# Optimization experiments

Hardware: AMD Instinct MI355X
Metric: run time of the kernel (lower is better)

## Reference

```python
import jax, jax.numpy as jnp
import numpy as np
import math

C = 512
D = C // 4  # 128
SCALE = math.sqrt(D)

def setup_inputs() -> dict:
    key = jax.random.key(0)
    k1, k2, k3, k4 = jax.random.split(key, 4)
    x = jax.random.normal(k1, (8, C, 2048), dtype=jnp.float32)
    # q_conv and k_conv share the same weight (tied in the torch module)
    wqk = jax.random.normal(k2, (D, C), dtype=jnp.float32) * (1.0 / math.sqrt(C))
    wv = jax.random.normal(k3, (D, C), dtype=jnp.float32) * (1.0 / math.sqrt(C))
    bv = jax.random.normal(k4, (D,), dtype=jnp.float32) * 0.01
    return {"x": x, "wqk": wqk, "wv": wv, "bv": bv}

def reference(x, wqk, wv, bv):
    # x: [B, C, N]; 1x1 conv == matmul over channel dim
    xq = jnp.einsum('dc,bcn->bnd', wqk, x)          # [B, N, D]
    xk = jnp.einsum('dc,bcn->bdn', wqk, x)          # [B, D, N]
    xv = jnp.einsum('dc,bcn->bdn', wv, x) + bv[None, :, None]  # [B, D, N]
    energy = jnp.einsum('bnd,bdm->bnm', xq, xk) / SCALE  # [B, N, N]
    attention = jax.nn.softmax(energy, axis=-1)
    x_r = jnp.einsum('bdn,bnm->bdm', xv, attention)  # [B, D, N]
    return x_r
```

## Files before the change

### kernel.cpp

```cpp
#include <hip/hip_runtime.h>

typedef short short4v __attribute__((ext_vector_type(4)));
typedef short short8 __attribute__((ext_vector_type(8)));
typedef float floatx4 __attribute__((ext_vector_type(4)));
typedef unsigned int uint;
typedef unsigned short ushort;

#define CH 512
#define NN 2048
#define DD 128
#define RSCALE 0.08838834764831845f

__device__ __forceinline__ float bf2f(ushort u) {
    union { uint i; float f; } v; v.i = ((uint)u) << 16; return v.f;
}
__device__ __forceinline__ ushort f2bf(float f) {
    union { float f; uint u; } v; v.f = f;
    uint u = v.u;
    return (ushort)((u + 0x7fffu + ((u >> 16) & 1u)) >> 16);
}

__global__ __launch_bounds__(256) void k0_prep(
    const float* __restrict__ wqk, const float* __restrict__ wv,
    ushort* __restrict__ Wbf, float* __restrict__ lsum)
{
    int gid = blockIdx.x * 256 + threadIdx.x;
    int base = gid * 4;
    const float* src = (base < 65536) ? (wqk + base) : (wv + base - 65536);
    float4 v = *(const float4*)src;
    short4v o;
    o[0] = (short)f2bf(v.x); o[1] = (short)f2bf(v.y);
    o[2] = (short)f2bf(v.z); o[3] = (short)f2bf(v.w);
    *(short4v*)&Wbf[base] = o;
    if (gid < 16384) lsum[gid] = 0.0f;
}

__global__ __launch_bounds__(256) void k1_proj(
    const float* __restrict__ x,
    const ushort* __restrict__ Wbf,
    const float* __restrict__ bv,
    ushort* __restrict__ Q,
    ushort* __restrict__ V)
{
    const int nt = blockIdx.x;
    const int b  = blockIdx.y;
    const int n0 = nt * 32;
    const int t = threadIdx.x;
    const int lane = t & 63, w = t >> 6, l15 = lane & 15, quad = lane >> 4;

    __shared__ __attribute__((aligned(16))) ushort As[32 * 40];
    __shared__ __attribute__((aligned(16))) ushort Bs[256 * 40];

    floatx4 acc[2][4];
#pragma unroll
    for (int i = 0; i < 2; i++)
#pragma unroll
        for (int j = 0; j < 4; j++) acc[i][j] = (floatx4)(0.0f);

    const float* xb = x + b * (CH * NN) + n0;

    for (int c0 = 0; c0 < CH; c0 += 32) {
        {
            int n = t & 31, g = t >> 5;
            short4v v;
#pragma unroll
            for (int i = 0; i < 4; i++)
                v[i] = (short)f2bf(xb[(c0 + g * 4 + i) * NN + n]);
            *(short4v*)&As[n * 40 + g * 4] = v;
        }
#pragma unroll
        for (int rep = 0; rep < 16; rep++) {
            int idx = rep * 256 + t;
            int row = idx >> 4, cp = idx & 15;
            *(uint*)&Bs[row * 40 + cp * 2] = *(const uint*)&Wbf[row * CH + c0 + cp * 2];
        }
        __syncthreads();
        short8 a0 = *(short8*)&As[(l15) * 40 + quad * 8];
        short8 a1 = *(short8*)&As[(16 + l15) * 40 + quad * 8];
#pragma unroll
        for (int dt2 = 0; dt2 < 4; dt2++) {
            short8 bf = *(short8*)&Bs[(w * 64 + dt2 * 16 + l15) * 40 + quad * 8];
            acc[0][dt2] = __builtin_amdgcn_mfma_f32_16x16x32_bf16(a0, bf, acc[0][dt2], 0, 0, 0);
            acc[1][dt2] = __builtin_amdgcn_mfma_f32_16x16x32_bf16(a1, bf, acc[1][dt2], 0, 0, 0);
        }
        __syncthreads();
    }
#pragma unroll
    for (int ns = 0; ns < 2; ns++)
#pragma unroll
        for (int dt2 = 0; dt2 < 4; dt2++) {
            int ds_ = w * 64 + dt2 * 16 + l15;
#pragma unroll
            for (int r = 0; r < 4; r++) {
                int n = n0 + ns * 16 + quad * 4 + r;
                float val = acc[ns][dt2][r];
                if (ds_ < 128) {
                    Q[b * (NN * DD) + n * DD + ds_] = f2bf(val);
                } else {
                    int dv = ds_ - 128;
                    V[b * (NN * DD) + n * DD + dv] = f2bf(val + bv[dv]);
                }
            }
        }
}

__global__ __launch_bounds__(256) void kl_sum(
    const ushort* __restrict__ Q,
    float* __restrict__ lsum)
{
    int pid = blockIdx.x;
    const int b = blockIdx.y;
    int it = 0;
    while (pid >= (16 - it)) { pid -= (16 - it); it++; }
    const int jt = it + pid;
    const int i0 = it * 128, j0 = jt * 128;
    const int t = threadIdx.x;
    const int lane = t & 63, w = t >> 6, l15 = lane & 15, quad = lane >> 4;
    const int wi = (w >> 1) * 64, wj = (w & 1) * 64;

    __shared__ __attribute__((aligned(16))) ushort Qi[128 * 136];
    __shared__ __attribute__((aligned(16))) ushort Qj[128 * 136];

    const ushort* Qb = Q + b * (NN * DD);

#pragma unroll
    for (int rep = 0; rep < 8; rep++) {
        int idx = rep * 256 + t;
        int row = idx >> 4, g = idx & 15;
        *(short8*)&Qi[row * 136 + g * 8] = *(const short8*)&Qb[(i0 + row) * DD + g * 8];
        *(short8*)&Qj[row * 136 + g * 8] = *(const short8*)&Qb[(j0 + row) * DD + g * 8];
    }
    __syncthreads();

    floatx4 acc[4][4];
#pragma unroll
    for (int i = 0; i < 4; i++)
#pragma unroll
        for (int j = 0; j < 4; j++) acc[i][j] = (floatx4)(0.0f);

#pragma unroll
    for (int kd = 0; kd < 4; kd++) {
        short8 afr[4], bfr[4];
#pragma unroll
        for (int nt = 0; nt < 4; nt++)
            afr[nt] = *(short8*)&Qi[(wi + nt * 16 + l15) * 136 + kd * 32 + quad * 8];
#pragma unroll
        for (int mt = 0; mt < 4; mt++)
            bfr[mt] = *(short8*)&Qj[(wj + mt * 16 + l15) * 136 + kd * 32 + quad * 8];
#pragma unroll
        for (int nt = 0; nt < 4; nt++)
#pragma unroll
            for (int mt = 0; mt < 4; mt++)
                acc[nt][mt] = __builtin_amdgcn_mfma_f32_16x16x32_bf16(afr[nt], bfr[mt], acc[nt][mt], 0, 0, 0);
    }

    float cs[4] = {0.f, 0.f, 0.f, 0.f};
#pragma unroll
    for (int nt = 0; nt < 4; nt++) {
        float rs[4] = {0.f, 0.f, 0.f, 0.f};
#pragma unroll
        for (int mt = 0; mt < 4; mt++)
#pragma unroll
            for (int r = 0; r < 4; r++) {
                float p = __expf(acc[nt][mt][r] * RSCALE);
                rs[r] += p;
                cs[mt] += p;
            }
#pragma unroll
        for (int r = 0; r < 4; r++) {
            float s = rs[r];
            s += __shfl_xor(s, 1);
            s += __shfl_xor(s, 2);
            s += __shfl_xor(s, 4);
            s += __shfl_xor(s, 8);
            if (l15 == 0)
                atomicAdd(&lsum[b * NN + i0 + wi + nt * 16 + quad * 4 + r], s);
        }
    }
    if (it != jt) {
#pragma unroll
        for (int mt = 0; mt < 4; mt++) {
            float s = cs[mt];
            s += __shfl_xor(s, 16);
            s += __shfl_xor(s, 32);
            if (lane < 16)
                atomicAdd(&lsum[b * NN + j0 + wj + mt * 16 + l15], s);
        }
    }
}

__global__ __launch_bounds__(256) void k2_scale_t(
    const ushort* __restrict__ V,
    const float* __restrict__ lsum,
    ushort* __restrict__ VT)
{
    const int nt = blockIdx.x;
    const int b = blockIdx.y;
    const int n0 = nt * 64;
    const int t = threadIdx.x;

    __shared__ __attribute__((aligned(16))) ushort Vt[64 * 132];

    const ushort* Vb = V + b * (NN * DD);
#pragma unroll
    for (int rep = 0; rep < 16; rep++) {
        int idx = rep * 256 + t;
        int row = idx >> 6, dp = idx & 63;
        *(uint*)&Vt[row * 132 + dp * 2] = *(const uint*)&Vb[(n0 + row) * DD + dp * 2];
    }
    __syncthreads();
#pragma unroll
    for (int rep = 0; rep < 16; rep++) {
        int idx = rep * 256 + t;
        int d = idx >> 5, col2 = idx & 31;
        int n = n0 + col2 * 2;
        float l0 = 1.0f / lsum[b * NN + n], l1 = 1.0f / lsum[b * NN + n + 1];
        float v0 = bf2f(Vt[(col2 * 2) * 132 + d]) * l0;
        float v1 = bf2f(Vt[(col2 * 2 + 1) * 132 + d]) * l1;
        uint pack = (uint)f2bf(v0) | ((uint)f2bf(v1) << 16);
        *(uint*)&VT[(size_t)b * DD * NN + (size_t)d * NN + n] = pack;
    }
}

__global__ __launch_bounds__(256) void k_fused(
    const ushort* __restrict__ Q,
    const ushort* __restrict__ VT,
    float* __restrict__ part)
{
    const int mt = blockIdx.x;
    const int h  = blockIdx.y;
    const int b  = blockIdx.z;
    const int m0 = mt * 64;
    const int t = threadIdx.x;
    const int lane = t & 63, w = t >> 6, l15 = lane & 15, quad = lane >> 4;

    __shared__ __attribute__((aligned(16))) ushort Qm[64 * 136];
    __shared__ __attribute__((aligned(16))) ushort Qn[64 * 136];
    __shared__ __attribute__((aligned(16))) ushort Vs[128 * 72];
    __shared__ __attribute__((aligned(16))) ushort Ps[64 * 68];

    const ushort* Qb = Q + b * (NN * DD);
    const ushort* VTb = VT + (size_t)b * DD * NN;

#pragma unroll
    for (int rep = 0; rep < 4; rep++) {
        int idx = rep * 256 + t;
        int row = idx >> 4, g = idx & 15;
        *(short8*)&Qm[row * 136 + g * 8] = *(const short8*)&Qb[(m0 + row) * DD + g * 8];
    }
    __syncthreads();

    short8 qm[4][4];
#pragma unroll
    for (int ms = 0; ms < 4; ms++)
#pragma unroll
        for (int kd = 0; kd < 4; kd++)
            qm[ms][kd] = *(short8*)&Qm[(ms * 16 + l15) * 136 + kd * 32 + quad * 8];

    floatx4 acc[2][4];
#pragma unroll
    for (int i = 0; i < 2; i++)
#pragma unroll
        for (int j = 0; j < 4; j++) acc[i][j] = (floatx4)(0.0f);

    const int nbeg = h * (NN / 2), nend = nbeg + (NN / 2);
    for (int n0c = nbeg; n0c < nend; n0c += 64) {
        __syncthreads();
#pragma unroll
        for (int rep = 0; rep < 4; rep++) {
            int idx = rep * 256 + t;
            int row = idx >> 4, g = idx & 15;
            *(short8*)&Qn[row * 136 + g * 8] = *(const short8*)&Qb[(n0c + row) * DD + g * 8];
        }
#pragma unroll
        for (int rep = 0; rep < 4; rep++) {
            int idx = rep * 256 + t;
            int d = idx >> 3, g = idx & 7;
            *(short8*)&Vs[d * 72 + g * 8] = *(const short8*)&VTb[(size_t)d * NN + n0c + g * 8];
        }
        __syncthreads();

        {
            short8 bq[4];
#pragma unroll
            for (int kd = 0; kd < 4; kd++)
                bq[kd] = *(short8*)&Qn[(w * 16 + l15) * 136 + kd * 32 + quad * 8];
#pragma unroll
            for (int ms = 0; ms < 4; ms++) {
                floatx4 s = (floatx4)(0.0f);
#pragma unroll
                for (int kd = 0; kd < 4; kd++)
                    s = __builtin_amdgcn_mfma_f32_16x16x32_bf16(qm[ms][kd], bq[kd], s, 0, 0, 0);
#pragma unroll
                for (int r = 0; r < 4; r++) {
                    float p = __expf(s[r] * RSCALE);
                    Ps[(ms * 16 + quad * 4 + r) * 68 + w * 16 + l15] = f2bf(p);
                }
            }
        }
        __syncthreads();

#pragma unroll
        for (int kn = 0; kn < 2; kn++) {
            short8 va0 = *(short8*)&Vs[(w * 32 + l15) * 72 + kn * 32 + quad * 8];
            short8 va1 = *(short8*)&Vs[(w * 32 + 16 + l15) * 72 + kn * 32 + quad * 8];
#pragma unroll
            for (int mf = 0; mf < 4; mf++) {
                short8 pb = *(short8*)&Ps[(mf * 16 + l15) * 68 + kn * 32 + quad * 8];
                acc[0][mf] = __builtin_amdgcn_mfma_f32_16x16x32_bf16(va0, pb, acc[0][mf], 0, 0, 0);
                acc[1][mf] = __builtin_amdgcn_mfma_f32_16x16x32_bf16(va1, pb, acc[1][mf], 0, 0, 0);
            }
        }
    }

    float* ob = part + (size_t)h * (8 * DD * NN) + (size_t)b * DD * NN;
#pragma unroll
    for (int dsub = 0; dsub < 2; dsub++)
#pragma unroll
        for (int mf = 0; mf < 4; mf++)
#pragma unroll
            for (int r = 0; r < 4; r++) {
                int d = w * 32 + dsub * 16 + quad * 4 + r;
                ob[(size_t)d * NN + m0 + mf * 16 + l15] = acc[dsub][mf][r];
            }
}

__global__ __launch_bounds__(256) void k_reduce(
    const float* __restrict__ part, float* __restrict__ out)
{
    int gid = blockIdx.x * 256 + threadIdx.x;
    const size_t half = (size_t)8 * DD * NN;
    float4 a = *(const float4*)&part[gid * 4];
    float4 b = *(const float4*)&part[half + gid * 4];
    float4 o;
    o.x = a.x + b.x; o.y = a.y + b.y; o.z = a.z + b.z; o.w = a.w + b.w;
    *(float4*)&out[gid * 4] = o;
}

__global__ __launch_bounds__(256) void k1_fb(
    const float* __restrict__ x, const float* __restrict__ wqk,
    const float* __restrict__ wv, const float* __restrict__ bv,
    ushort* __restrict__ Q, ushort* __restrict__ V)
{
    const int nt = blockIdx.x;
    const int b  = blockIdx.y;
    const int n0 = nt * 32;
    const int t = threadIdx.x;
    const int lane = t & 63, w = t >> 6, l15 = lane & 15, quad = lane >> 4;

    __shared__ __attribute__((aligned(16))) ushort As[32 * 40];
    __shared__ __attribute__((aligned(16))) ushort Bs[256 * 40];

    floatx4 acc[2][4];
#pragma unroll
    for (int i = 0; i < 2; i++)
#pragma unroll
        for (int j = 0; j < 4; j++) acc[i][j] = (floatx4)(0.0f);

    const float* xb = x + b * (CH * NN) + n0;

    for (int c0 = 0; c0 < CH; c0 += 32) {
        {
            int n = t & 31, g = t >> 5;
            short4v v;
#pragma unroll
            for (int i = 0; i < 4; i++)
                v[i] = (short)f2bf(xb[(c0 + g * 4 + i) * NN + n]);
            *(short4v*)&As[n * 40 + g * 4] = v;
        }
#pragma unroll
        for (int rep = 0; rep < 16; rep++) {
            int idx = rep * 256 + t;
            int row = idx >> 4, cp = idx & 15;
            const float* wf = (row < 128) ? (wqk + row * CH) : (wv + (row - 128) * CH);
            uint pack = (uint)f2bf(wf[c0 + cp * 2]) | ((uint)f2bf(wf[c0 + cp * 2 + 1]) << 16);
            *(uint*)&Bs[row * 40 + cp * 2] = pack;
        }
        __syncthreads();
        short8 a0 = *(short8*)&As[(l15) * 40 + quad * 8];
        short8 a1 = *(short8*)&As[(16 + l15) * 40 + quad * 8];
#pragma unroll
        for (int dt2 = 0; dt2 < 4; dt2++) {
            short8 bf = *(short8*)&Bs[(w * 64 + dt2 * 16 + l15) * 40 + quad * 8];
            acc[0][dt2] = __builtin_amdgcn_mfma_f32_16x16x32_bf16(a0, bf, acc[0][dt2], 0, 0, 0);
            acc[1][dt2] = __builtin_amdgcn_mfma_f32_16x16x32_bf16(a1, bf, acc[1][dt2], 0, 0, 0);
        }
        __syncthreads();
    }
#pragma unroll
    for (int ns = 0; ns < 2; ns++)
#pragma unroll
        for (int dt2 = 0; dt2 < 4; dt2++) {
            int ds_ = w * 64 + dt2 * 16 + l15;
#pragma unroll
            for (int r = 0; r < 4; r++) {
                int n = n0 + ns * 16 + quad * 4 + r;
                float val = acc[ns][dt2][r];
                if (ds_ < 128) {
                    Q[b * (NN * DD) + n * DD + ds_] = f2bf(val);
                } else {
                    int dv = ds_ - 128;
                    V[b * (NN * DD) + n * DD + dv] = f2bf(val + bv[dv]);
                }
            }
        }
}

__global__ __launch_bounds__(256) void k2_norm(
    const ushort* __restrict__ Q, ushort* __restrict__ V)
{
    const int ntile = blockIdx.x;
    const int b = blockIdx.y;
    const int n0 = ntile * 64;
    const int t = threadIdx.x;
    const int lane = t & 63, w = t >> 6, l15 = lane & 15, quad = lane >> 4;

    __shared__ __attribute__((aligned(16))) ushort Qs[64 * 136];
    __shared__ __attribute__((aligned(16))) ushort Qm2[64 * 136];

    const ushort* Qb = Q + b * (NN * DD);

#pragma unroll
    for (int rep = 0; rep < 16; rep++) {
        int idx = rep * 256 + t;
        int row = idx >> 6, dp = idx & 63;
        *(uint*)&Qs[row * 136 + dp * 2] = *(const uint*)&Qb[(n0 + row) * DD + dp * 2];
    }
    __syncthreads();

    short8 afr[4];
#pragma unroll
    for (int kd = 0; kd < 4; kd++)
        afr[kd] = *(short8*)&Qs[(w * 16 + l15) * 136 + kd * 32 + quad * 8];

    float sums[4] = {0.f, 0.f, 0.f, 0.f};

    for (int m0 = 0; m0 < NN; m0 += 64) {
#pragma unroll
        for (int rep = 0; rep < 16; rep++) {
            int idx = rep * 256 + t;
            int row = idx >> 6, dp = idx & 63;
            *(uint*)&Qm2[row * 136 + dp * 2] = *(const uint*)&Qb[(m0 + row) * DD + dp * 2];
        }
        __syncthreads();
#pragma unroll
        for (int ct = 0; ct < 4; ct++) {
            floatx4 s = (floatx4)(0.0f);
#pragma unroll
            for (int kd = 0; kd < 4; kd++) {
                short8 bf = *(short8*)&Qm2[(ct * 16 + l15) * 136 + kd * 32 + quad * 8];
                s = __builtin_amdgcn_mfma_f32_16x16x32_bf16(afr[kd], bf, s, 0, 0, 0);
            }
#pragma unroll
            for (int r = 0; r < 4; r++)
                sums[r] += __expf(s[r] * RSCALE);
        }
        __syncthreads();
    }

#pragma unroll
    for (int r = 0; r < 4; r++) {
        float s = sums[r];
        s += __shfl_xor(s, 1);
        s += __shfl_xor(s, 2);
        s += __shfl_xor(s, 4);
        s += __shfl_xor(s, 8);
        sums[r] = s;
    }

    ushort* Vb = V + b * (NN * DD);
#pragma unroll
    for (int r = 0; r < 4; r++) {
        int n = n0 + w * 16 + quad * 4 + r;
        float inv = 1.0f / sums[r];
        short8 vv = *(short8*)&Vb[n * DD + l15 * 8];
        short8 o;
#pragma unroll
        for (int i = 0; i < 8; i++)
            o[i] = (short)f2bf(bf2f((ushort)vv[i]) * inv);
        *(short8*)&Vb[n * DD + l15 * 8] = o;
    }
}

__global__ __launch_bounds__(256) void k3_attn(
    const ushort* __restrict__ Q, const ushort* __restrict__ Vp,
    float* __restrict__ out)
{
    const int mtile = blockIdx.x;
    const int b = blockIdx.y;
    const int m0 = mtile * 64;
    const int t = threadIdx.x;
    const int lane = t & 63, w = t >> 6, l15 = lane & 15, quad = lane >> 4;

    __shared__ __attribute__((aligned(16))) ushort Qs[64 * 136];
    __shared__ __attribute__((aligned(16))) ushort Qn2[32 * 136];
    __shared__ __attribute__((aligned(16))) ushort Vs2[128 * 40];
    __shared__ __attribute__((aligned(16))) ushort Ps2[64 * 40];

    const ushort* Qb = Q + b * (NN * DD);
    const ushort* Vpb = Vp + b * (NN * DD);

#pragma unroll
    for (int rep = 0; rep < 16; rep++) {
        int idx = rep * 256 + t;
        int row = idx >> 6, dp = idx & 63;
        *(uint*)&Qs[row * 136 + dp * 2] = *(const uint*)&Qb[(m0 + row) * DD + dp * 2];
    }
    __syncthreads();

    short8 afr[4];
#pragma unroll
    for (int kd = 0; kd < 4; kd++)
        afr[kd] = *(short8*)&Qs[(w * 16 + l15) * 136 + kd * 32 + quad * 8];

    floatx4 acc[2][4];
#pragma unroll
    for (int s = 0; s < 2; s++)
#pragma unroll
        for (int mt = 0; mt < 4; mt++) acc[s][mt] = (floatx4)(0.0f);

    for (int n0c = 0; n0c < NN; n0c += 32) {
#pragma unroll
        for (int rep = 0; rep < 8; rep++) {
            int idx = rep * 256 + t;
            int row = idx >> 6, dp = idx & 63;
            *(uint*)&Qn2[row * 136 + dp * 2] = *(const uint*)&Qb[(n0c + row) * DD + dp * 2];
        }
#pragma unroll
        for (int rep = 0; rep < 8; rep++) {
            int idx = rep * 256 + t;
            int np = idx >> 7, d = idx & 127;
            uint v0 = Vpb[(n0c + np * 2) * DD + d];
            uint v1 = Vpb[(n0c + np * 2 + 1) * DD + d];
            *(uint*)&Vs2[d * 40 + np * 2] = v0 | (v1 << 16);
        }
        __syncthreads();

#pragma unroll
        for (int nt2 = 0; nt2 < 2; nt2++) {
            floatx4 s = (floatx4)(0.0f);
#pragma unroll
            for (int kd = 0; kd < 4; kd++) {
                short8 bf = *(short8*)&Qn2[(nt2 * 16 + l15) * 136 + kd * 32 + quad * 8];
                s = __builtin_amdgcn_mfma_f32_16x16x32_bf16(afr[kd], bf, s, 0, 0, 0);
            }
#pragma unroll
            for (int r = 0; r < 4; r++) {
                float p = __expf(s[r] * RSCALE);
                Ps2[(w * 16 + quad * 4 + r) * 40 + nt2 * 16 + l15] = f2bf(p);
            }
        }
        __syncthreads();

        short8 pb[4];
#pragma unroll
        for (int mt = 0; mt < 4; mt++)
            pb[mt] = *(short8*)&Ps2[(mt * 16 + l15) * 40 + quad * 8];
#pragma unroll
        for (int sub = 0; sub < 2; sub++) {
            short8 va = *(short8*)&Vs2[(w * 32 + sub * 16 + l15) * 40 + quad * 8];
#pragma unroll
            for (int mt = 0; mt < 4; mt++)
                acc[sub][mt] = __builtin_amdgcn_mfma_f32_16x16x32_bf16(va, pb[mt], acc[sub][mt], 0, 0, 0);
        }
        __syncthreads();
    }

    float* ob = out + (size_t)b * DD * NN;
#pragma unroll
    for (int sub = 0; sub < 2; sub++)
#pragma unroll
        for (int mt = 0; mt < 4; mt++)
#pragma unroll
            for (int r = 0; r < 4; r++) {
                int d = w * 32 + sub * 16 + quad * 4 + r;
                int m = m0 + mt * 16 + l15;
                ob[(size_t)d * NN + m] = acc[sub][mt][r];
            }
}

extern "C" void kernel_launch(void* const* d_in, const int* in_sizes, int n_in,
                              void* d_out, int out_size, void* d_ws, size_t ws_size,
                              hipStream_t stream) {
    const float* x   = (const float*)d_in[0];
    const float* wqk = (const float*)d_in[1];
    const float* wv  = (const float*)d_in[2];
    const float* bv  = (const float*)d_in[3];
    float* out = (float*)d_out;

    ushort* Q = (ushort*)d_ws;
    ushort* V = (ushort*)((char*)d_ws + (4u << 20));

    if (ws_size >= (size_t)33 * 1024 * 1024) {
        ushort* Wbf  = (ushort*)((char*)d_ws + (8u << 20));
        float*  lsum = (float*)((char*)d_ws + (8u << 20) + (256u << 10));
        ushort* VT   = (ushort*)((char*)d_ws + (12u << 20));
        float*  part = (float*)((char*)d_ws + (16u << 20));

        k0_prep<<<128, 256, 0, stream>>>(wqk, wv, Wbf, lsum);
        k1_proj<<<dim3(64, 8), 256, 0, stream>>>(x, Wbf, bv, Q, V);
        kl_sum<<<dim3(136, 8), 256, 0, stream>>>(Q, lsum);
        k2_scale_t<<<dim3(32, 8), 256, 0, stream>>>(V, lsum, VT);
        k_fused<<<dim3(32, 2, 8), 256, 0, stream>>>(Q, VT, part);
        k_reduce<<<2048, 256, 0, stream>>>(part, out);
    } else {
        k1_fb<<<dim3(64, 8), 256, 0, stream>>>(x, wqk, wv, bv, Q, V);
        k2_norm<<<dim3(32, 8), 256, 0, stream>>>(Q, V);
        k3_attn<<<dim3(32, 8), 256, 0, stream>>>(Q, V, out);
    }
}
```

Measured before the change: 156.5 us.

## Write V transposed from projection and fold softmax normalization into fused attention

Result: faster. 152.2 us (-2.7%).

```diff
diff --git a/kernel.cpp b/kernel.cpp
--- a/kernel.cpp
+++ b/kernel.cpp
@@ -40,7 +40,7 @@
     const ushort* __restrict__ Wbf,
     const float* __restrict__ bv,
     ushort* __restrict__ Q,
-    ushort* __restrict__ V)
+    ushort* __restrict__ VT)
 {
     const int nt = blockIdx.x;
     const int b  = blockIdx.y;
@@ -50,6 +50,7 @@
 
     __shared__ __attribute__((aligned(16))) ushort As[32 * 40];
     __shared__ __attribute__((aligned(16))) ushort Bs[256 * 40];
+    __shared__ __attribute__((aligned(16))) ushort Vt[128 * 40];
 
     floatx4 acc[2][4];
 #pragma unroll
@@ -69,10 +70,292 @@
             *(short4v*)&As[n * 40 + g * 4] = v;
         }
 #pragma unroll
+        for (int rep = 0; rep < 4; rep++) {
+            int idx = rep * 256 + t;
+            int row = idx >> 2, g = idx & 3;
+            *(short8*)&Bs[row * 40 + g * 8] = *(const short8*)&Wbf[row * CH + c0 + g * 8];
+        }
+        __syncthreads();
+        short8 a0 = *(short8*)&As[(l15) * 40 + quad * 8];
+        short8 a1 = *(short8*)&As[(16 + l15) * 40 + quad * 8];
+#pragma unroll
+        for (int dt2 = 0; dt2 < 4; dt2++) {
+            short8 bf = *(short8*)&Bs[(w * 64 + dt2 * 16 + l15) * 40 + quad * 8];
+            acc[0][dt2] = __builtin_amdgcn_mfma_f32_16x16x32_bf16(a0, bf, acc[0][dt2], 0, 0, 0);
+            acc[1][dt2] = __builtin_amdgcn_mfma_f32_16x16x32_bf16(a1, bf, acc[1][dt2], 0, 0, 0);
+        }
+        __syncthreads();
+    }
+
+#pragma unroll
+    for (int ns = 0; ns < 2; ns++)
+#pragma unroll
+        for (int dt2 = 0; dt2 < 4; dt2++) {
+            int ds_ = w * 64 + dt2 * 16 + l15;
+#pragma unroll
+            for (int r = 0; r < 4; r++) {
+                int nl = ns * 16 + quad * 4 + r;
+                float val = acc[ns][dt2][r];
+                if (ds_ < 128) {
+                    Q[b * (NN * DD) + (n0 + nl) * DD + ds_] = f2bf(val);
+                } else {
+                    int dv = ds_ - 128;
+                    Vt[dv * 40 + nl] = f2bf(val + bv[dv]);
+                }
+            }
+        }
+    __syncthreads();
+#pragma unroll
+    for (int rep = 0; rep < 2; rep++) {
+        int idx = rep * 256 + t;
+        int dv = idx >> 2, seg = idx & 3;
+        *(short8*)&VT[((size_t)b * DD + dv) * NN + n0 + seg * 8] =
+            *(short8*)&Vt[dv * 40 + seg * 8];
+    }
+}
+
+__global__ __launch_bounds__(256) void kl_sum(
+    const ushort* __restrict__ Q,
+    float* __restrict__ lsum)
+{
+    int pid = blockIdx.x;
+    const int b = blockIdx.y;
+    int it = 0;
+    while (pid >= (16 - it)) { pid -= (16 - it); it++; }
+    const int jt = it + pid;
+    const int i0 = it * 128, j0 = jt * 128;
+    const int t = threadIdx.x;
+    const int lane = t & 63, w = t >> 6, l15 = lane & 15, quad = lane >> 4;
+    const int wi = (w >> 1) * 64, wj = (w & 1) * 64;
+
+    __shared__ __attribute__((aligned(16))) ushort Qi[128 * 136];
+    __shared__ __attribute__((aligned(16))) ushort Qj[128 * 136];
+
+    const ushort* Qb = Q + b * (NN * DD);
+
+#pragma unroll
+    for (int rep = 0; rep < 8; rep++) {
+        int idx = rep * 256 + t;
+        int row = idx >> 4, g = idx & 15;
+        *(short8*)&Qi[row * 136 + g * 8] = *(const short8*)&Qb[(i0 + row) * DD + g * 8];
+        *(short8*)&Qj[row * 136 + g * 8] = *(const short8*)&Qb[(j0 + row) * DD + g * 8];
+    }
+    __syncthreads();
+
+    floatx4 acc[4][4];
+#pragma unroll
+    for (int i = 0; i < 4; i++)
+#pragma unroll
+        for (int j = 0; j < 4; j++) acc[i][j] = (floatx4)(0.0f);
+
+#pragma unroll
+    for (int kd = 0; kd < 4; kd++) {
+        short8 afr[4], bfr[4];
+#pragma unroll
+        for (int nt = 0; nt < 4; nt++)
+            afr[nt] = *(short8*)&Qi[(wi + nt * 16 + l15) * 136 + kd * 32 + quad * 8];
+#pragma unroll
+        for (int mt = 0; mt < 4; mt++)
+            bfr[mt] = *(short8*)&Qj[(wj + mt * 16 + l15) * 136 + kd * 32 + quad * 8];
+#pragma unroll
+        for (int nt = 0; nt < 4; nt++)
+#pragma unroll
+            for (int mt = 0; mt < 4; mt++)
+                acc[nt][mt] = __builtin_amdgcn_mfma_f32_16x16x32_bf16(afr[nt], bfr[mt], acc[nt][mt], 0, 0, 0);
+    }
+
+    float cs[4] = {0.f, 0.f, 0.f, 0.f};
+#pragma unroll
+    for (int nt = 0; nt < 4; nt++) {
+        float rs[4] = {0.f, 0.f, 0.f, 0.f};
+#pragma unroll
+        for (int mt = 0; mt < 4; mt++)
+#pragma unroll
+            for (int r = 0; r < 4; r++) {
+                float p = __expf(acc[nt][mt][r] * RSCALE);
+                rs[r] += p;
+                cs[mt] += p;
+            }
+#pragma unroll
+        for (int r = 0; r < 4; r++) {
+            float s = rs[r];
+            s += __shfl_xor(s, 1);
+            s += __shfl_xor(s, 2);
+            s += __shfl_xor(s, 4);
+            s += __shfl_xor(s, 8);
+            if (l15 == 0)
+                atomicAdd(&lsum[b * NN + i0 + wi + nt * 16 + quad * 4 + r], s);
+        }
+    }
+    if (it != jt) {
+#pragma unroll
+        for (int mt = 0; mt < 4; mt++) {
+            float s = cs[mt];
+            s += __shfl_xor(s, 16);
+            s += __shfl_xor(s, 32);
+            if (lane < 16)
+                atomicAdd(&lsum[b * NN + j0 + wj + mt * 16 + l15], s);
+        }
+    }
+}
+
+__global__ __launch_bounds__(256) void k_fused(
+    const ushort* __restrict__ Q,
+    const ushort* __restrict__ VT,
+    const float* __restrict__ lsum,
+    float* __restrict__ part)
+{
+    const int mt = blockIdx.x;
+    const int h  = blockIdx.y;
+    const int b  = blockIdx.z;
+    const int m0 = mt * 64;
+    const int t = threadIdx.x;
+    const int lane = t & 63, w = t >> 6, l15 = lane & 15, quad = lane >> 4;
+
+    __shared__ __attribute__((aligned(16))) ushort Qm[64 * 136];
+    __shared__ __attribute__((aligned(16))) ushort Qn[64 * 136];
+    __shared__ __attribute__((aligned(16))) ushort Vs[128 * 72];
+    __shared__ __attribute__((aligned(16))) ushort Ps[64 * 68];
+
+    const ushort* Qb = Q + b * (NN * DD);
+    const ushort* VTb = VT + (size_t)b * DD * NN;
+    const float* lb = lsum + b * NN;
+
+#pragma unroll
+    for (int rep = 0; rep < 4; rep++) {
+        int idx = rep * 256 + t;
+        int row = idx >> 4, g = idx & 15;
+        *(short8*)&Qm[row * 136 + g * 8] = *(const short8*)&Qb[(m0 + row) * DD + g * 8];
+    }
+    __syncthreads();
+
+    short8 qm[4][4];
+#pragma unroll
+    for (int ms = 0; ms < 4; ms++)
+#pragma unroll
+        for (int kd = 0; kd < 4; kd++)
+            qm[ms][kd] = *(short8*)&Qm[(ms * 16 + l15) * 136 + kd * 32 + quad * 8];
+
+    floatx4 acc[2][4];
+#pragma unroll
+    for (int i = 0; i < 2; i++)
+#pragma unroll
+        for (int j = 0; j < 4; j++) acc[i][j] = (floatx4)(0.0f);
+
+    const int nbeg = h * (NN / 2), nend = nbeg + (NN / 2);
+    for (int n0c = nbeg; n0c < nend; n0c += 64) {
+        float lw = lb[n0c + w * 16 + l15];
+        __syncthreads();
+#pragma unroll
+        for (int rep = 0; rep < 4; rep++) {
+            int idx = rep * 256 + t;
+            int row = idx >> 4, g = idx & 15;
+            *(short8*)&Qn[row * 136 + g * 8] = *(const short8*)&Qb[(n0c + row) * DD + g * 8];
+        }
+#pragma unroll
+        for (int rep = 0; rep < 4; rep++) {
+            int idx = rep * 256 + t;
+            int d = idx >> 3, g = idx & 7;
+            *(short8*)&Vs[d * 72 + g * 8] = *(const short8*)&VTb[(size_t)d * NN + n0c + g * 8];
+        }
+        __syncthreads();
+
+        {
+            float linv = 1.0f / lw;
+            short8 bq[4];
+#pragma unroll
+            for (int kd = 0; kd < 4; kd++)
+                bq[kd] = *(short8*)&Qn[(w * 16 + l15) * 136 + kd * 32 + quad * 8];
+#pragma unroll
+            for (int ms = 0; ms < 4; ms++) {
+                floatx4 s = (floatx4)(0.0f);
+#pragma unroll
+                for (int kd = 0; kd < 4; kd++)
+                    s = __builtin_amdgcn_mfma_f32_16x16x32_bf16(qm[ms][kd], bq[kd], s, 0, 0, 0);
+#pragma unroll
+                for (int r = 0; r < 4; r++) {
+                    float p = __expf(s[r] * RSCALE) * linv;
+                    Ps[(ms * 16 + quad * 4 + r) * 68 + w * 16 + l15] = f2bf(p);
+                }
+            }
+        }
+        __syncthreads();
+
+#pragma unroll
+        for (int kn = 0; kn < 2; kn++) {
+            short8 va0 = *(short8*)&Vs[(w * 32 + l15) * 72 + kn * 32 + quad * 8];
+            short8 va1 = *(short8*)&Vs[(w * 32 + 16 + l15) * 72 + kn * 32 + quad * 8];
+#pragma unroll
+            for (int mf = 0; mf < 4; mf++) {
+                short8 pb = *(short8*)&Ps[(mf * 16 + l15) * 68 + kn * 32 + quad * 8];
+                acc[0][mf] = __builtin_amdgcn_mfma_f32_16x16x32_bf16(va0, pb, acc[0][mf], 0, 0, 0);
+                acc[1][mf] = __builtin_amdgcn_mfma_f32_16x16x32_bf16(va1, pb, acc[1][mf], 0, 0, 0);
+            }
+        }
+    }
+
+    float* ob = part + (size_t)h * (8 * DD * NN) + (size_t)b * DD * NN;
+#pragma unroll
+    for (int dsub = 0; dsub < 2; dsub++)
+#pragma unroll
+        for (int mf = 0; mf < 4; mf++)
+#pragma unroll
+            for (int r = 0; r < 4; r++) {
+                int d = w * 32 + dsub * 16 + quad * 4 + r;
+                ob[(size_t)d * NN + m0 + mf * 16 + l15] = acc[dsub][mf][r];
+            }
+}
+
+__global__ __launch_bounds__(256) void k_reduce(
+    const float* __restrict__ part, float* __restrict__ out)
+{
+    int gid = blockIdx.x * 256 + threadIdx.x;
+    const size_t half = (size_t)8 * DD * NN;
+    float4 a = *(const float4*)&part[gid * 4];
+    float4 b = *(const float4*)&part[half + gid * 4];
+    float4 o;
+    o.x = a.x + b.x; o.y = a.y + b.y; o.z = a.z + b.z; o.w = a.w + b.w;
+    *(float4*)&out[gid * 4] = o;
+}
+
+__global__ __launch_bounds__(256) void k1_fb(
+    const float* __restrict__ x, const float* __restrict__ wqk,
+    const float* __restrict__ wv, const float* __restrict__ bv,
+    ushort* __restrict__ Q, ushort* __restrict__ V)
+{
+    const int nt = blockIdx.x;
+    const int b  = blockIdx.y;
+    const int n0 = nt * 32;
+    const int t = threadIdx.x;
+    const int lane = t & 63, w = t >> 6, l15 = lane & 15, quad = lane >> 4;
+
+    __shared__ __attribute__((aligned(16))) ushort As[32 * 40];
+    __shared__ __attribute__((aligned(16))) ushort Bs[256 * 40];
+
+    floatx4 acc[2][4];
+#pragma unroll
+    for (int i = 0; i < 2; i++)
+#pragma unroll
+        for (int j = 0; j < 4; j++) acc[i][j] = (floatx4)(0.0f);
+
+    const float* xb = x + b * (CH * NN) + n0;
+
+    for (int c0 = 0; c0 < CH; c0 += 32) {
+        {
+            int n = t & 31, g = t >> 5;
+            short4v v;
+#pragma unroll
+            for (int i = 0; i < 4; i++)
+                v[i] = (short)f2bf(xb[(c0 + g * 4 + i) * NN + n]);
+            *(short4v*)&As[n * 40 + g * 4] = v;
+        }
+#pragma unroll
         for (int rep = 0; rep < 16; rep++) {
             int idx = rep * 256 + t;
             int row = idx >> 4, cp = idx & 15;
-            *(uint*)&Bs[row * 40 + cp * 2] = *(const uint*)&Wbf[row * CH + c0 + cp * 2];
+            const float* wf = (row < 128) ? (wqk + row * CH) : (wv + (row - 128) * CH);
+            uint pack = (uint)f2bf(wf[c0 + cp * 2]) | ((uint)f2bf(wf[c0 + cp * 2 + 1]) << 16);
+            *(uint*)&Bs[row * 40 + cp * 2] = pack;
         }
         __syncthreads();
         short8 a0 = *(short8*)&As[(l15) * 40 + quad * 8];
@@ -104,308 +387,6 @@
         }
 }
 
-__global__ __launch_bounds__(256) void kl_sum(
-    const ushort* __restrict__ Q,
-    float* __restrict__ lsum)
-{
-    int pid = blockIdx.x;
-    const int b = blockIdx.y;
-    int it = 0;
-    while (pid >= (16 - it)) { pid -= (16 - it); it++; }
-    const int jt = it + pid;
-    const int i0 = it * 128, j0 = jt * 128;
-    const int t = threadIdx.x;
-    const int lane = t & 63, w = t >> 6, l15 = lane & 15, quad = lane >> 4;
-    const int wi = (w >> 1) * 64, wj = (w & 1) * 64;
-
-    __shared__ __attribute__((aligned(16))) ushort Qi[128 * 136];
-    __shared__ __attribute__((aligned(16))) ushort Qj[128 * 136];
-
-    const ushort* Qb = Q + b * (NN * DD);
-
-#pragma unroll
-    for (int rep = 0; rep < 8; rep++) {
-        int idx = rep * 256 + t;
-        int row = idx >> 4, g = idx & 15;
-        *(short8*)&Qi[row * 136 + g * 8] = *(const short8*)&Qb[(i0 + row) * DD + g * 8];
-        *(short8*)&Qj[row * 136 + g * 8] = *(const short8*)&Qb[(j0 + row) * DD + g * 8];
-    }
-    __syncthreads();
-
-    floatx4 acc[4][4];
-#pragma unroll
-    for (int i = 0; i < 4; i++)
-#pragma unroll
-        for (int j = 0; j < 4; j++) acc[i][j] = (floatx4)(0.0f);
-
-#pragma unroll
-    for (int kd = 0; kd < 4; kd++) {
-        short8 afr[4], bfr[4];
-#pragma unroll
-        for (int nt = 0; nt < 4; nt++)
-            afr[nt] = *(short8*)&Qi[(wi + nt * 16 + l15) * 136 + kd * 32 + quad * 8];
-#pragma unroll
-        for (int mt = 0; mt < 4; mt++)
-            bfr[mt] = *(short8*)&Qj[(wj + mt * 16 + l15) * 136 + kd * 32 + quad * 8];
-#pragma unroll
-        for (int nt = 0; nt < 4; nt++)
-#pragma unroll
-            for (int mt = 0; mt < 4; mt++)
-                acc[nt][mt] = __builtin_amdgcn_mfma_f32_16x16x32_bf16(afr[nt], bfr[mt], acc[nt][mt], 0, 0, 0);
-    }
-
-    float cs[4] = {0.f, 0.f, 0.f, 0.f};
-#pragma unroll
-    for (int nt = 0; nt < 4; nt++) {
-        float rs[4] = {0.f, 0.f, 0.f, 0.f};
-#pragma unroll
-        for (int mt = 0; mt < 4; mt++)
-#pragma unroll
-            for (int r = 0; r < 4; r++) {
-                float p = __expf(acc[nt][mt][r] * RSCALE);
-                rs[r] += p;
-                cs[mt] += p;
-            }
-#pragma unroll
-        for (int r = 0; r < 4; r++) {
-            float s = rs[r];
-            s += __shfl_xor(s, 1);
-            s += __shfl_xor(s, 2);
-            s += __shfl_xor(s, 4);
-            s += __shfl_xor(s, 8);
-            if (l15 == 0)
-                atomicAdd(&lsum[b * NN + i0 + wi + nt * 16 + quad * 4 + r], s);
-        }
-    }
-    if (it != jt) {
-#pragma unroll
-        for (int mt = 0; mt < 4; mt++) {
-            float s = cs[mt];
-            s += __shfl_xor(s, 16);
-            s += __shfl_xor(s, 32);
-            if (lane < 16)
-                atomicAdd(&lsum[b * NN + j0 + wj + mt * 16 + l15], s);
-        }
-    }
-}
-
-__global__ __launch_bounds__(256) void k2_scale_t(
-    const ushort* __restrict__ V,
-    const float* __restrict__ lsum,
-    ushort* __restrict__ VT)
-{
-    const int nt = blockIdx.x;
-    const int b = blockIdx.y;
-    const int n0 = nt * 64;
-    const int t = threadIdx.x;
-
-    __shared__ __attribute__((aligned(16))) ushort Vt[64 * 132];
-
-    const ushort* Vb = V + b * (NN * DD);
-#pragma unroll
-    for (int rep = 0; rep < 16; rep++) {
-        int idx = rep * 256 + t;
-        int row = idx >> 6, dp = idx & 63;
-        *(uint*)&Vt[row * 132 + dp * 2] = *(const uint*)&Vb[(n0 + row) * DD + dp * 2];
-    }
-    __syncthreads();
-#pragma unroll
-    for (int rep = 0; rep < 16; rep++) {
-        int idx = rep * 256 + t;
-        int d = idx >> 5, col2 = idx & 31;
-        int n = n0 + col2 * 2;
-        float l0 = 1.0f / lsum[b * NN + n], l1 = 1.0f / lsum[b * NN + n + 1];
-        float v0 = bf2f(Vt[(col2 * 2) * 132 + d]) * l0;
-        float v1 = bf2f(Vt[(col2 * 2 + 1) * 132 + d]) * l1;
-        uint pack = (uint)f2bf(v0) | ((uint)f2bf(v1) << 16);
-        *(uint*)&VT[(size_t)b * DD * NN + (size_t)d * NN + n] = pack;
-    }
-}
-
-__global__ __launch_bounds__(256) void k_fused(
-    const ushort* __restrict__ Q,
-    const ushort* __restrict__ VT,
-    float* __restrict__ part)
-{
-    const int mt = blockIdx.x;
-    const int h  = blockIdx.y;
-    const int b  = blockIdx.z;
-    const int m0 = mt * 64;
-    const int t = threadIdx.x;
-    const int lane = t & 63, w = t >> 6, l15 = lane & 15, quad = lane >> 4;
-
-    __shared__ __attribute__((aligned(16))) ushort Qm[64 * 136];
-    __shared__ __attribute__((aligned(16))) ushort Qn[64 * 136];
-    __shared__ __attribute__((aligned(16))) ushort Vs[128 * 72];
-    __shared__ __attribute__((aligned(16))) ushort Ps[64 * 68];
-
-    const ushort* Qb = Q + b * (NN * DD);
-    const ushort* VTb = VT + (size_t)b * DD * NN;
-
-#pragma unroll
-    for (int rep = 0; rep < 4; rep++) {
-        int idx = rep * 256 + t;
-        int row = idx >> 4, g = idx & 15;
-        *(short8*)&Qm[row * 136 + g * 8] = *(const short8*)&Qb[(m0 + row) * DD + g * 8];
-    }
-    __syncthreads();
-
-    short8 qm[4][4];
-#pragma unroll
-    for (int ms = 0; ms < 4; ms++)
-#pragma unroll
-        for (int kd = 0; kd < 4; kd++)
-            qm[ms][kd] = *(short8*)&Qm[(ms * 16 + l15) * 136 + kd * 32 + quad * 8];
-
-    floatx4 acc[2][4];
-#pragma unroll
-    for (int i = 0; i < 2; i++)
-#pragma unroll
-        for (int j = 0; j < 4; j++) acc[i][j] = (floatx4)(0.0f);
-
-    const int nbeg = h * (NN / 2), nend = nbeg + (NN / 2);
-    for (int n0c = nbeg; n0c < nend; n0c += 64) {
-        __syncthreads();
-#pragma unroll
-        for (int rep = 0; rep < 4; rep++) {
-            int idx = rep * 256 + t;
-            int row = idx >> 4, g = idx & 15;
-            *(short8*)&Qn[row * 136 + g * 8] = *(const short8*)&Qb[(n0c + row) * DD + g * 8];
-        }
-#pragma unroll
-        for (int rep = 0; rep < 4; rep++) {
-            int idx = rep * 256 + t;
-            int d = idx >> 3, g = idx & 7;
-            *(short8*)&Vs[d * 72 + g * 8] = *(const short8*)&VTb[(size_t)d * NN + n0c + g * 8];
-        }
-        __syncthreads();
-
-        {
-            short8 bq[4];
-#pragma unroll
-            for (int kd = 0; kd < 4; kd++)
-                bq[kd] = *(short8*)&Qn[(w * 16 + l15) * 136 + kd * 32 + quad * 8];
-#pragma unroll
-            for (int ms = 0; ms < 4; ms++) {
-                floatx4 s = (floatx4)(0.0f);
-#pragma unroll
-                for (int kd = 0; kd < 4; kd++)
-                    s = __builtin_amdgcn_mfma_f32_16x16x32_bf16(qm[ms][kd], bq[kd], s, 0, 0, 0);
-#pragma unroll
-                for (int r = 0; r < 4; r++) {
-                    float p = __expf(s[r] * RSCALE);
-                    Ps[(ms * 16 + quad * 4 + r) * 68 + w * 16 + l15] = f2bf(p);
-                }
-            }
-        }
-        __syncthreads();
-
-#pragma unroll
-        for (int kn = 0; kn < 2; kn++) {
-            short8 va0 = *(short8*)&Vs[(w * 32 + l15) * 72 + kn * 32 + quad * 8];
-            short8 va1 = *(short8*)&Vs[(w * 32 + 16 + l15) * 72 + kn * 32 + quad * 8];
-#pragma unroll
-            for (int mf = 0; mf < 4; mf++) {
-                short8 pb = *(short8*)&Ps[(mf * 16 + l15) * 68 + kn * 32 + quad * 8];
-                acc[0][mf] = __builtin_amdgcn_mfma_f32_16x16x32_bf16(va0, pb, acc[0][mf], 0, 0, 0);
-                acc[1][mf] = __builtin_amdgcn_mfma_f32_16x16x32_bf16(va1, pb, acc[1][mf], 0, 0, 0);
-            }
-        }
-    }
-
-    float* ob = part + (size_t)h * (8 * DD * NN) + (size_t)b * DD * NN;
-#pragma unroll
-    for (int dsub = 0; dsub < 2; dsub++)
-#pragma unroll
-        for (int mf = 0; mf < 4; mf++)
-#pragma unroll
-            for (int r = 0; r < 4; r++) {
-                int d = w * 32 + dsub * 16 + quad * 4 + r;
-                ob[(size_t)d * NN + m0 + mf * 16 + l15] = acc[dsub][mf][r];
-            }
-}
-
-__global__ __launch_bounds__(256) void k_reduce(
-    const float* __restrict__ part, float* __restrict__ out)
-{
-    int gid = blockIdx.x * 256 + threadIdx.x;
-    const size_t half = (size_t)8 * DD * NN;
-    float4 a = *(const float4*)&part[gid * 4];
-    float4 b = *(const float4*)&part[half + gid * 4];
-    float4 o;
-    o.x = a.x + b.x; o.y = a.y + b.y; o.z = a.z + b.z; o.w = a.w + b.w;
-    *(float4*)&out[gid * 4] = o;
-}
-
-__global__ __launch_bounds__(256) void k1_fb(
-    const float* __restrict__ x, const float* __restrict__ wqk,
-    const float* __restrict__ wv, const float* __restrict__ bv,
-    ushort* __restrict__ Q, ushort* __restrict__ V)
-{
-    const int nt = blockIdx.x;
-    const int b  = blockIdx.y;
-    const int n0 = nt * 32;
-    const int t = threadIdx.x;
-    const int lane = t & 63, w = t >> 6, l15 = lane & 15, quad = lane >> 4;
-
-    __shared__ __attribute__((aligned(16))) ushort As[32 * 40];
-    __shared__ __attribute__((aligned(16))) ushort Bs[256 * 40];
-
-    floatx4 acc[2][4];
-#pragma unroll
-    for (int i = 0; i < 2; i++)
-#pragma unroll
-        for (int j = 0; j < 4; j++) acc[i][j] = (floatx4)(0.0f);
-
-    const float* xb = x + b * (CH * NN) + n0;
-
-    for (int c0 = 0; c0 < CH; c0 += 32) {
-        {
-            int n = t & 31, g = t >> 5;
-            short4v v;
-#pragma unroll
-            for (int i = 0; i < 4; i++)
-                v[i] = (short)f2bf(xb[(c0 + g * 4 + i) * NN + n]);
-            *(short4v*)&As[n * 40 + g * 4] = v;
-        }
-#pragma unroll
-        for (int rep = 0; rep < 16; rep++) {
-            int idx = rep * 256 + t;
-            int row = idx >> 4, cp = idx & 15;
-            const float* wf = (row < 128) ? (wqk + row * CH) : (wv + (row - 128) * CH);
-            uint pack = (uint)f2bf(wf[c0 + cp * 2]) | ((uint)f2bf(wf[c0 + cp * 2 + 1]) << 16);
-            *(uint*)&Bs[row * 40 + cp * 2] = pack;
-        }
-        __syncthreads();
-        short8 a0 = *(short8*)&As[(l15) * 40 + quad * 8];
-        short8 a1 = *(short8*)&As[(16 + l15) * 40 + quad * 8];
-#pragma unroll
-        for (int dt2 = 0; dt2 < 4; dt2++) {
-            short8 bf = *(short8*)&Bs[(w * 64 + dt2 * 16 + l15) * 40 + quad * 8];
-            acc[0][dt2] = __builtin_amdgcn_mfma_f32_16x16x32_bf16(a0, bf, acc[0][dt2], 0, 0, 0);
-            acc[1][dt2] = __builtin_amdgcn_mfma_f32_16x16x32_bf16(a1, bf, acc[1][dt2], 0, 0, 0);
-        }
-        __syncthreads();
-    }
-#pragma unroll
-    for (int ns = 0; ns < 2; ns++)
-#pragma unroll
-        for (int dt2 = 0; dt2 < 4; dt2++) {
-            int ds_ = w * 64 + dt2 * 16 + l15;
-#pragma unroll
-            for (int r = 0; r < 4; r++) {
-                int n = n0 + ns * 16 + quad * 4 + r;
-                float val = acc[ns][dt2][r];
-                if (ds_ < 128) {
-                    Q[b * (NN * DD) + n * DD + ds_] = f2bf(val);
-                } else {
-                    int dv = ds_ - 128;
-                    V[b * (NN * DD) + n * DD + dv] = f2bf(val + bv[dv]);
-                }
-            }
-        }
-}
-
 __global__ __launch_bounds__(256) void k2_norm(
     const ushort* __restrict__ Q, ushort* __restrict__ V)
 {
@@ -589,21 +570,20 @@
     float* out = (float*)d_out;
 
     ushort* Q = (ushort*)d_ws;
-    ushort* V = (ushort*)((char*)d_ws + (4u << 20));
 
     if (ws_size >= (size_t)33 * 1024 * 1024) {
+        ushort* VT   = (ushort*)((char*)d_ws + (4u << 20));
         ushort* Wbf  = (ushort*)((char*)d_ws + (8u << 20));
         float*  lsum = (float*)((char*)d_ws + (8u << 20) + (256u << 10));
-        ushort* VT   = (ushort*)((char*)d_ws + (12u << 20));
         float*  part = (float*)((char*)d_ws + (16u << 20));
 
         k0_prep<<<128, 256, 0, stream>>>(wqk, wv, Wbf, lsum);
-        k1_proj<<<dim3(64, 8), 256, 0, stream>>>(x, Wbf, bv, Q, V);
+        k1_proj<<<dim3(64, 8), 256, 0, stream>>>(x, Wbf, bv, Q, VT);
         kl_sum<<<dim3(136, 8), 256, 0, stream>>>(Q, lsum);
-        k2_scale_t<<<dim3(32, 8), 256, 0, stream>>>(V, lsum, VT);
-        k_fused<<<dim3(32, 2, 8), 256, 0, stream>>>(Q, VT, part);
+        k_fused<<<dim3(32, 2, 8), 256, 0, stream>>>(Q, VT, lsum, part);
         k_reduce<<<2048, 256, 0, stream>>>(part, out);
     } else {
+        ushort* V = (ushort*)((char*)d_ws + (4u << 20));
         k1_fb<<<dim3(64, 8), 256, 0, stream>>>(x, wqk, wv, bv, Q, V);
         k2_norm<<<dim3(32, 8), 256, 0, stream>>>(Q, V);
         k3_attn<<<dim3(32, 8), 256, 0, stream>>>(Q, V, out);
```
